# Optimization experiments

Measured on AMD Instinct MI355X. Metric: run time of the kernel, lower is better.

Reference implementation:

```python
import jax, jax.numpy as jnp
import numpy as np

DIM = 512

def setup_inputs() -> dict:
    key = jax.random.key(0)
    kx, kq, kk, kv = jax.random.split(key, 4)
    x = jax.random.normal(kx, (8, 2048, DIM), dtype=jnp.float32)
    # Dense kernels are [in_dim, out_dim], no bias
    Wq = jax.random.normal(kq, (DIM, DIM), dtype=jnp.float32) * (DIM ** -0.5)
    Wk = jax.random.normal(kk, (DIM, DIM), dtype=jnp.float32) * (DIM ** -0.5)
    Wv = jax.random.normal(kv, (DIM, DIM), dtype=jnp.float32) * (DIM ** -0.5)
    return {"x": x, "Wq": Wq, "Wk": Wk, "Wv": Wv}

def reference(x, Wq, Wk, Wv):
    # x: [b, s, d]
    q = jnp.einsum('bsd,de->bse', x, Wq)
    k = jnp.einsum('bsd,de->bse', x, Wk)
    v = jnp.einsum('bsd,de->bse', x, Wv)
    scale = jnp.sqrt(jnp.asarray(DIM, dtype=x.dtype))
    attn = jnp.einsum('bqe,bke->bqk', q, k) / scale  # [b, s, s]
    attn = jax.nn.softmax(attn, axis=-1)
    return jnp.einsum('bqk,bke->bqe', attn, v)  # [b, s, d]
```

## Files before the change

kernel.cpp:

```cpp
#include <hip/hip_runtime.h>
#include <stdint.h>

typedef unsigned short u16;
typedef unsigned int u32;
typedef float floatx4 __attribute__((ext_vector_type(4)));
typedef __bf16 bf16x8 __attribute__((ext_vector_type(8)));
typedef __attribute__((address_space(1))) const u32 gu32;
typedef __attribute__((address_space(3))) u32 lu32;

#define SEQ 2048
#define DIM 512
#define NBATCH 8

__device__ __forceinline__ u16 f2bf(float f) {
  u32 u = __float_as_uint(f);
  u += 0x7fffu + ((u >> 16) & 1u);
  return (u16)(u >> 16);
}

__device__ __forceinline__ void stage_tile64(const u16* __restrict__ g, int ld, int k0, u16* lds) {
  const int t = threadIdx.x;
  const int wave = t >> 6, lane = t & 63;
  const int rsub = lane >> 3;
  const int lg = (lane & 7) ^ rsub;
#pragma unroll
  for (int q = 0; q < 4; ++q) {
    const int chunk = wave * 4 + q;
    const int row = chunk * 8 + rsub;
    const u16* gp = g + (size_t)row * ld + k0 + lg * 8;
    u16* lp = lds + chunk * 512 + lane * 8;
    __builtin_amdgcn_global_load_lds((gu32*)gp, (lu32*)lp, 16, 0, 0);
  }
}

__device__ __forceinline__ void gemm_core(const u16* A, const u16* BT, int lda, int ldb, int kdim,
                                          u16* As, u16* Bs, floatx4 acc[4][4]) {
  const int t = threadIdx.x;
  const int wave = t >> 6, lane = t & 63;
  const int wr = (wave >> 1) * 64, wc = (wave & 1) * 64;
  const int l15 = lane & 15, quad = lane >> 4;
  const int swz = l15 & 7;
  for (int k0 = 0; k0 < kdim; k0 += 64) {
    stage_tile64(A, lda, k0, As);
    stage_tile64(BT, ldb, k0, Bs);
    __syncthreads();
#pragma unroll
    for (int ks = 0; ks < 2; ++ks) {
      const int pg = ((ks << 2) + quad) ^ swz;
      bf16x8 af[4], bfr[4];
#pragma unroll
      for (int i = 0; i < 4; ++i) {
        af[i]  = *(const bf16x8*)(As + (wr + i * 16 + l15) * 64 + pg * 8);
        bfr[i] = *(const bf16x8*)(Bs + (wc + i * 16 + l15) * 64 + pg * 8);
      }
#pragma unroll
      for (int mi = 0; mi < 4; ++mi)
#pragma unroll
        for (int ni = 0; ni < 4; ++ni)
          acc[mi][ni] = __builtin_amdgcn_mfma_f32_16x16x32_bf16(af[mi], bfr[ni], acc[mi][ni], 0, 0, 0);
    }
    __syncthreads();
  }
}

__device__ __forceinline__ void zero_acc(floatx4 acc[4][4]) {
#pragma unroll
  for (int i = 0; i < 4; ++i)
#pragma unroll
    for (int j = 0; j < 4; ++j)
      acc[i][j] = (floatx4){0.f, 0.f, 0.f, 0.f};
}

__global__ __launch_bounds__(256) void k_cvt_x(const float* __restrict__ x, u16* __restrict__ xb) {
  size_t i = ((size_t)blockIdx.x * 256 + threadIdx.x) * 8;
  float4 a = *(const float4*)(x + i);
  float4 b = *(const float4*)(x + i + 4);
  u16 o[8] = {f2bf(a.x), f2bf(a.y), f2bf(a.z), f2bf(a.w),
              f2bf(b.x), f2bf(b.y), f2bf(b.z), f2bf(b.w)};
  *(uint4*)(xb + i) = *(const uint4*)o;
}

__global__ __launch_bounds__(256) void k_pack_w(const float* __restrict__ Wq, const float* __restrict__ Wk,
                                                const float* __restrict__ Wv, u16* __restrict__ wt) {
  int t = blockIdx.x * 256 + threadIdx.x;
  int k = t & 511, n = t >> 9;
  int sec = n >> 9, nc = n & 511;
  const float* W = (sec == 0) ? Wq : (sec == 1) ? Wk : Wv;
  wt[(size_t)n * 512 + k] = f2bf(W[(size_t)k * 512 + nc]);
}

__global__ __launch_bounds__(256) void k_qkv(const u16* __restrict__ xb, const u16* __restrict__ wt,
                                             u16* __restrict__ qo, u16* __restrict__ ko,
                                             u16* __restrict__ vt) {
  __shared__ __align__(16) u16 As[128 * 64];
  __shared__ __align__(16) u16 Bs[128 * 64];
  const int m0 = blockIdx.x * 128, n0 = blockIdx.y * 128;
  floatx4 acc[4][4];
  zero_acc(acc);
  gemm_core(xb + (size_t)m0 * DIM, wt + (size_t)n0 * DIM, DIM, DIM, DIM, As, Bs, acc);
  const int t = threadIdx.x, wave = t >> 6, lane = t & 63;
  const int wr = (wave >> 1) * 64, wc = (wave & 1) * 64;
  const int l15 = lane & 15, quad = lane >> 4;
  const int sec = n0 >> 9;
#pragma unroll
  for (int mi = 0; mi < 4; ++mi)
#pragma unroll
    for (int ni = 0; ni < 4; ++ni)
#pragma unroll
      for (int r = 0; r < 4; ++r) {
        int m = m0 + wr + mi * 16 + quad * 4 + r;
        int n = n0 + wc + ni * 16 + l15;
        float v = acc[mi][ni][r];
        int nc = n & 511;
        if (sec == 0) {
          qo[(size_t)m * DIM + nc] = f2bf(v * 0.04419417382415922f);
        } else if (sec == 1) {
          ko[(size_t)m * DIM + nc] = f2bf(v);
        } else {
          int b = m >> 11, s = m & 2047;
          vt[((size_t)(b * DIM + nc)) * SEQ + s] = f2bf(v);
        }
      }
}

__global__ __launch_bounds__(256) void k_scores(const u16* __restrict__ q, const u16* __restrict__ kk,
                                                u16* __restrict__ sc, float* __restrict__ rowsum,
                                                int b0) {
  __shared__ __align__(16) u16 As[128 * 64];
  __shared__ __align__(16) u16 Bs[128 * 64];
  const int bz = blockIdx.z, bb = b0 + bz;
  const int m0 = blockIdx.x * 128, n0 = blockIdx.y * 128;
  floatx4 acc[4][4];
  zero_acc(acc);
  gemm_core(q + (size_t)bb * SEQ * DIM + (size_t)m0 * DIM,
            kk + (size_t)bb * SEQ * DIM + (size_t)n0 * DIM, DIM, DIM, DIM, As, Bs, acc);
  u16* C = sc + (size_t)bz * SEQ * SEQ;
  float* rsb = rowsum + (size_t)bb * SEQ;
  const int t = threadIdx.x, wave = t >> 6, lane = t & 63;
  const int wr = (wave >> 1) * 64, wc = (wave & 1) * 64;
  const int l15 = lane & 15, quad = lane >> 4;
#pragma unroll
  for (int mi = 0; mi < 4; ++mi)
#pragma unroll
    for (int r = 0; r < 4; ++r) {
      int m = m0 + wr + mi * 16 + quad * 4 + r;
      float p = 0.f;
#pragma unroll
      for (int ni = 0; ni < 4; ++ni) {
        int n = n0 + wc + ni * 16 + l15;
        float e = __expf(acc[mi][ni][r]);
        C[(size_t)m * SEQ + n] = f2bf(e);
        p += e;
      }
      p += __shfl_xor(p, 1); p += __shfl_xor(p, 2);
      p += __shfl_xor(p, 4); p += __shfl_xor(p, 8);
      if (l15 == 0) atomicAdd(&rsb[m], p);
    }
}

__global__ __launch_bounds__(256) void k_pv(const u16* __restrict__ sc, const u16* __restrict__ vt,
                                            const float* __restrict__ rowsum,
                                            float* __restrict__ out, int b0) {
  __shared__ __align__(16) u16 As[128 * 64];
  __shared__ __align__(16) u16 Bs[128 * 64];
  const int bz = blockIdx.z, bb = b0 + bz;
  const int m0 = blockIdx.x * 128, n0 = blockIdx.y * 128;
  floatx4 acc[4][4];
  zero_acc(acc);
  gemm_core(sc + (size_t)bz * SEQ * SEQ + (size_t)m0 * SEQ,
            vt + (size_t)bb * DIM * SEQ + (size_t)n0 * SEQ, SEQ, SEQ, SEQ, As, Bs, acc);
  float* C = out + (size_t)bb * SEQ * DIM;
  const float* rsb = rowsum + (size_t)bb * SEQ;
  const int t = threadIdx.x, wave = t >> 6, lane = t & 63;
  const int wr = (wave >> 1) * 64, wc = (wave & 1) * 64;
  const int l15 = lane & 15, quad = lane >> 4;
#pragma unroll
  for (int mi = 0; mi < 4; ++mi)
#pragma unroll
    for (int r = 0; r < 4; ++r) {
      int m = m0 + wr + mi * 16 + quad * 4 + r;
      float inv = 1.0f / rsb[m];
#pragma unroll
      for (int ni = 0; ni < 4; ++ni) {
        int n = n0 + wc + ni * 16 + l15;
        C[(size_t)m * DIM + n] = acc[mi][ni][r] * inv;
      }
    }
}

extern "C" void kernel_launch(void* const* d_in, const int* in_sizes, int n_in,
                              void* d_out, int out_size, void* d_ws, size_t ws_size,
                              hipStream_t stream) {
  const float* x  = (const float*)d_in[0];
  const float* Wq = (const float*)d_in[1];
  const float* Wk = (const float*)d_in[2];
  const float* Wv = (const float*)d_in[3];
  float* out = (float*)d_out;
  char* ws = (char*)d_ws;

  u16* xb   = (u16*)(ws + 0);
  u16* wt   = (u16*)(ws + 16777216);
  u16* qo   = (u16*)(ws + 18350080);
  u16* ko   = (u16*)(ws + 35127296);
  u16* vt   = (u16*)(ws + 51904512);
  float* rs = (float*)(ws + 68681728);
  u16* sc   = (u16*)(ws + 68747264);
  const size_t base_need = 68747264;
  const size_t per_b = (size_t)SEQ * SEQ * 2;
  size_t avail = (ws_size > base_need) ? (ws_size - base_need) : 0;
  int nb = (int)(avail / per_b);
  if (nb < 1) nb = 1;
  if (nb > NBATCH) nb = NBATCH;

  hipMemsetAsync(rs, 0, (size_t)NBATCH * SEQ * sizeof(float), stream);
  k_cvt_x<<<dim3(4096), dim3(256), 0, stream>>>(x, xb);
  k_pack_w<<<dim3(3072), dim3(256), 0, stream>>>(Wq, Wk, Wv, wt);
  k_qkv<<<dim3(128, 12), dim3(256), 0, stream>>>(xb, wt, qo, ko, vt);
  for (int b0 = 0; b0 < NBATCH; b0 += nb) {
    int nbr = (NBATCH - b0 < nb) ? (NBATCH - b0) : nb;
    k_scores<<<dim3(16, 16, nbr), dim3(256), 0, stream>>>(qo, ko, sc, rs, b0);
    k_pv<<<dim3(16, 4, nbr), dim3(256), 0, stream>>>(sc, vt, rs, out, b0);
  }
}
```

Baseline: 248.7 us.

## Enlarge GEMM tiles to 256x256 with 8 waves; transpose weights via LDS

All three GEMM kernels (QKV projection, scores, PV) move from 128x128 tiles with 4 waves to 256x256 tiles with 8 waves, each wave computing a 128x64 sub-tile. The aim is more data reuse per LDS load and fewer global reads per FLOP. Weight packing now transposes through a shared-memory tile with vectorized loads and stores instead of strided scalar accesses. The cost is far fewer blocks: the PV kernel drops to 16 blocks per batch, which may leave many CUs idle. Each block also now needs 64KB of LDS and more registers.

```diff
diff --git a/kernel.cpp b/kernel.cpp
--- a/kernel.cpp
+++ b/kernel.cpp
@@ -18,7 +18,7 @@
   return (u16)(u >> 16);
 }
 
-__device__ __forceinline__ void stage_tile64(const u16* __restrict__ g, int ld, int k0, u16* lds) {
+__device__ __forceinline__ void stage256(const u16* __restrict__ g, int ld, int k0, u16* lds) {
   const int t = threadIdx.x;
   const int wave = t >> 6, lane = t & 63;
   const int rsub = lane >> 3;
@@ -34,27 +34,28 @@
 }
 
 __device__ __forceinline__ void gemm_core(const u16* A, const u16* BT, int lda, int ldb, int kdim,
-                                          u16* As, u16* Bs, floatx4 acc[4][4]) {
+                                          u16* As, u16* Bs, floatx4 acc[8][4]) {
   const int t = threadIdx.x;
   const int wave = t >> 6, lane = t & 63;
-  const int wr = (wave >> 1) * 64, wc = (wave & 1) * 64;
+  const int wr = (wave >> 2) * 128, wc = (wave & 3) * 64;
   const int l15 = lane & 15, quad = lane >> 4;
   const int swz = l15 & 7;
   for (int k0 = 0; k0 < kdim; k0 += 64) {
-    stage_tile64(A, lda, k0, As);
-    stage_tile64(BT, ldb, k0, Bs);
+    stage256(A, lda, k0, As);
+    stage256(BT, ldb, k0, Bs);
     __syncthreads();
 #pragma unroll
     for (int ks = 0; ks < 2; ++ks) {
       const int pg = ((ks << 2) + quad) ^ swz;
-      bf16x8 af[4], bfr[4];
-#pragma unroll
-      for (int i = 0; i < 4; ++i) {
+      bf16x8 af[8], bfr[4];
+#pragma unroll
+      for (int i = 0; i < 8; ++i)
         af[i]  = *(const bf16x8*)(As + (wr + i * 16 + l15) * 64 + pg * 8);
+#pragma unroll
+      for (int i = 0; i < 4; ++i)
         bfr[i] = *(const bf16x8*)(Bs + (wc + i * 16 + l15) * 64 + pg * 8);
-      }
-#pragma unroll
-      for (int mi = 0; mi < 4; ++mi)
+#pragma unroll
+      for (int mi = 0; mi < 8; ++mi)
 #pragma unroll
         for (int ni = 0; ni < 4; ++ni)
           acc[mi][ni] = __builtin_amdgcn_mfma_f32_16x16x32_bf16(af[mi], bfr[ni], acc[mi][ni], 0, 0, 0);
@@ -63,9 +64,9 @@
   }
 }
 
-__device__ __forceinline__ void zero_acc(floatx4 acc[4][4]) {
-#pragma unroll
-  for (int i = 0; i < 4; ++i)
+__device__ __forceinline__ void zero_acc(floatx4 acc[8][4]) {
+#pragma unroll
+  for (int i = 0; i < 8; ++i)
 #pragma unroll
     for (int j = 0; j < 4; ++j)
       acc[i][j] = (floatx4){0.f, 0.f, 0.f, 0.f};
@@ -82,28 +83,40 @@
 
 __global__ __launch_bounds__(256) void k_pack_w(const float* __restrict__ Wq, const float* __restrict__ Wk,
                                                 const float* __restrict__ Wv, u16* __restrict__ wt) {
-  int t = blockIdx.x * 256 + threadIdx.x;
-  int k = t & 511, n = t >> 9;
-  int sec = n >> 9, nc = n & 511;
+  __shared__ float tile[64][65];
+  const int t = threadIdx.x;
+  const int kb = blockIdx.x * 64, nb0 = blockIdx.y * 64, sec = blockIdx.z;
   const float* W = (sec == 0) ? Wq : (sec == 1) ? Wk : Wv;
-  wt[(size_t)n * 512 + k] = f2bf(W[(size_t)k * 512 + nc]);
-}
-
-__global__ __launch_bounds__(256) void k_qkv(const u16* __restrict__ xb, const u16* __restrict__ wt,
-                                             u16* __restrict__ qo, u16* __restrict__ ko,
-                                             u16* __restrict__ vt) {
-  __shared__ __align__(16) u16 As[128 * 64];
-  __shared__ __align__(16) u16 Bs[128 * 64];
-  const int m0 = blockIdx.x * 128, n0 = blockIdx.y * 128;
-  floatx4 acc[4][4];
+#pragma unroll
+  for (int i = 0; i < 4; ++i) {
+    int kr = i * 16 + (t >> 4), nc = (t & 15) * 4;
+    float4 v = *(const float4*)&W[(size_t)(kb + kr) * 512 + nb0 + nc];
+    tile[kr][nc] = v.x; tile[kr][nc + 1] = v.y; tile[kr][nc + 2] = v.z; tile[kr][nc + 3] = v.w;
+  }
+  __syncthreads();
+#pragma unroll
+  for (int i = 0; i < 4; ++i) {
+    int nr = i * 16 + (t >> 4), kc = (t & 15) * 4;
+    u16 o[4] = {f2bf(tile[kc][nr]), f2bf(tile[kc + 1][nr]), f2bf(tile[kc + 2][nr]), f2bf(tile[kc + 3][nr])};
+    *(uint2*)&wt[(size_t)(sec * 512 + nb0 + nr) * 512 + kb + kc] = *(const uint2*)o;
+  }
+}
+
+__global__ __launch_bounds__(512, 2) void k_qkv(const u16* __restrict__ xb, const u16* __restrict__ wt,
+                                                u16* __restrict__ qo, u16* __restrict__ ko,
+                                                u16* __restrict__ vt) {
+  __shared__ __align__(16) u16 As[256 * 64];
+  __shared__ __align__(16) u16 Bs[256 * 64];
+  const int m0 = blockIdx.x * 256, n0 = blockIdx.y * 256;
+  floatx4 acc[8][4];
   zero_acc(acc);
   gemm_core(xb + (size_t)m0 * DIM, wt + (size_t)n0 * DIM, DIM, DIM, DIM, As, Bs, acc);
   const int t = threadIdx.x, wave = t >> 6, lane = t & 63;
-  const int wr = (wave >> 1) * 64, wc = (wave & 1) * 64;
+  const int wr = (wave >> 2) * 128, wc = (wave & 3) * 64;
   const int l15 = lane & 15, quad = lane >> 4;
   const int sec = n0 >> 9;
 #pragma unroll
-  for (int mi = 0; mi < 4; ++mi)
+  for (int mi = 0; mi < 8; ++mi)
 #pragma unroll
     for (int ni = 0; ni < 4; ++ni)
 #pragma unroll
@@ -123,24 +136,24 @@
       }
 }
 
-__global__ __launch_bounds__(256) void k_scores(const u16* __restrict__ q, const u16* __restrict__ kk,
-                                                u16* __restrict__ sc, float* __restrict__ rowsum,
-                                                int b0) {
-  __shared__ __align__(16) u16 As[128 * 64];
-  __shared__ __align__(16) u16 Bs[128 * 64];
+__global__ __launch_bounds__(512, 2) void k_scores(const u16* __restrict__ q, const u16* __restrict__ kk,
+                                                   u16* __restrict__ sc, float* __restrict__ rowsum,
+                                                   int b0) {
+  __shared__ __align__(16) u16 As[256 * 64];
+  __shared__ __align__(16) u16 Bs[256 * 64];
   const int bz = blockIdx.z, bb = b0 + bz;
-  const int m0 = blockIdx.x * 128, n0 = blockIdx.y * 128;
-  floatx4 acc[4][4];
+  const int m0 = blockIdx.x * 256, n0 = blockIdx.y * 256;
+  floatx4 acc[8][4];
   zero_acc(acc);
   gemm_core(q + (size_t)bb * SEQ * DIM + (size_t)m0 * DIM,
             kk + (size_t)bb * SEQ * DIM + (size_t)n0 * DIM, DIM, DIM, DIM, As, Bs, acc);
   u16* C = sc + (size_t)bz * SEQ * SEQ;
   float* rsb = rowsum + (size_t)bb * SEQ;
   const int t = threadIdx.x, wave = t >> 6, lane = t & 63;
-  const int wr = (wave >> 1) * 64, wc = (wave & 1) * 64;
-  const int l15 = lane & 15, quad = lane >> 4;
-#pragma unroll
-  for (int mi = 0; mi < 4; ++mi)
+  const int wr = (wave >> 2) * 128, wc = (wave & 3) * 64;
+  const int l15 = lane & 15, quad = lane >> 4;
+#pragma unroll
+  for (int mi = 0; mi < 8; ++mi)
 #pragma unroll
     for (int r = 0; r < 4; ++r) {
       int m = m0 + wr + mi * 16 + quad * 4 + r;
@@ -158,24 +171,24 @@
     }
 }
 
-__global__ __launch_bounds__(256) void k_pv(const u16* __restrict__ sc, const u16* __restrict__ vt,
-                                            const float* __restrict__ rowsum,
-                                            float* __restrict__ out, int b0) {
-  __shared__ __align__(16) u16 As[128 * 64];
-  __shared__ __align__(16) u16 Bs[128 * 64];
+__global__ __launch_bounds__(512, 2) void k_pv(const u16* __restrict__ sc, const u16* __restrict__ vt,
+                                               const float* __restrict__ rowsum,
+                                               float* __restrict__ out, int b0) {
+  __shared__ __align__(16) u16 As[256 * 64];
+  __shared__ __align__(16) u16 Bs[256 * 64];
   const int bz = blockIdx.z, bb = b0 + bz;
-  const int m0 = blockIdx.x * 128, n0 = blockIdx.y * 128;
-  floatx4 acc[4][4];
+  const int m0 = blockIdx.x * 256, n0 = blockIdx.y * 256;
+  floatx4 acc[8][4];
   zero_acc(acc);
   gemm_core(sc + (size_t)bz * SEQ * SEQ + (size_t)m0 * SEQ,
             vt + (size_t)bb * DIM * SEQ + (size_t)n0 * SEQ, SEQ, SEQ, SEQ, As, Bs, acc);
   float* C = out + (size_t)bb * SEQ * DIM;
   const float* rsb = rowsum + (size_t)bb * SEQ;
   const int t = threadIdx.x, wave = t >> 6, lane = t & 63;
-  const int wr = (wave >> 1) * 64, wc = (wave & 1) * 64;
-  const int l15 = lane & 15, quad = lane >> 4;
-#pragma unroll
-  for (int mi = 0; mi < 4; ++mi)
+  const int wr = (wave >> 2) * 128, wc = (wave & 3) * 64;
+  const int l15 = lane & 15, quad = lane >> 4;
+#pragma unroll
+  for (int mi = 0; mi < 8; ++mi)
 #pragma unroll
     for (int r = 0; r < 4; ++r) {
       int m = m0 + wr + mi * 16 + quad * 4 + r;
@@ -214,11 +227,11 @@
 
   hipMemsetAsync(rs, 0, (size_t)NBATCH * SEQ * sizeof(float), stream);
   k_cvt_x<<<dim3(4096), dim3(256), 0, stream>>>(x, xb);
-  k_pack_w<<<dim3(3072), dim3(256), 0, stream>>>(Wq, Wk, Wv, wt);
-  k_qkv<<<dim3(128, 12), dim3(256), 0, stream>>>(xb, wt, qo, ko, vt);
+  k_pack_w<<<dim3(8, 8, 3), dim3(256), 0, stream>>>(Wq, Wk, Wv, wt);
+  k_qkv<<<dim3(64, 6), dim3(512), 0, stream>>>(xb, wt, qo, ko, vt);
   for (int b0 = 0; b0 < NBATCH; b0 += nb) {
     int nbr = (NBATCH - b0 < nb) ? (NBATCH - b0) : nb;
-    k_scores<<<dim3(16, 16, nbr), dim3(256), 0, stream>>>(qo, ko, sc, rs, b0);
-    k_pv<<<dim3(16, 4, nbr), dim3(256), 0, stream>>>(sc, vt, rs, out, b0);
-  }
-}
+    k_scores<<<dim3(8, 8, nbr), dim3(512), 0, stream>>>(qo, ko, sc, rs, b0);
+    k_pv<<<dim3(8, 2, nbr), dim3(512), 0, stream>>>(sc, vt, rs, out, b0);
+  }
+}
```

Result: slower. 290.0 us (+16.6%).
